# Kernel optimization log

Hardware: AMD Instinct MI355X
Metric: run time of the kernel (lower is better)

## Reference

```python
import jax, jax.numpy as jnp
import numpy as np

K = 20
EPS = 1e-5
SLOPE = 0.2

def _knn_idx(x, k):
    # x: [B, C, N] -> idx [B, N, k] of nearest neighbors (includes self)
    xx = jnp.sum(x * x, axis=1)                      # [B, N]
    inner = jnp.einsum('bcn,bcm->bnm', x, x)          # [B, N, N]
    dist = xx[:, :, None] - 2.0 * inner + xx[:, None, :]
    _, idx = jax.lax.top_k(-dist, k)                  # [B, N, k]
    return idx

def _get_attention_feature(x, k):
    # x: [B, C, N] -> [B, N, k, 2C] = cat([x_j - x_i, x_i])
    idx = _knn_idx(x, k)
    xt = jnp.transpose(x, (0, 2, 1))                  # [B, N, C]
    nbr = jax.vmap(lambda pts, ids: pts[ids])(xt, idx)  # [B, N, k, C]
    ctr = xt[:, :, None, :]                           # [B, N, 1, C]
    return jnp.concatenate([nbr - ctr, jnp.broadcast_to(ctr, nbr.shape)], axis=-1)

def _gat(feat, W, a):
    # feat: [B, N, k, 2C]; W: [2C, out_c]; a: [4, H] with H = out_c // 4
    B, N, k, _ = feat.shape
    out_c = W.shape[1]
    H = out_c // 4
    hw = jnp.einsum('bnkf,fd->bnkd', feat, W).reshape(B, N, k, H, 4)
    t = jax.nn.leaky_relu(hw, SLOPE)
    logits = jnp.einsum('bnkhd,dh->bnkh', t, a)
    w = jax.nn.softmax(logits, axis=2)                # softmax over neighbors k
    out = jnp.einsum('bnkh,bnkhd->bnhd', w, hw).reshape(B, N, out_c)
    out = jax.nn.leaky_relu(out, SLOPE)
    return jnp.transpose(out, (0, 2, 1))              # [B, out_c, N]

def _bn(x, gamma, beta):
    # BatchNorm1d in training mode (batch stats) over [B, C, N]
    mu = jnp.mean(x, axis=(0, 2), keepdims=True)
    var = jnp.var(x, axis=(0, 2), keepdims=True)
    xn = (x - mu) / jnp.sqrt(var + EPS)
    return xn * gamma[None, :, None] + beta[None, :, None]

def _layer(x, W, a, gamma, beta):
    feat = _get_attention_feature(x, K)
    h = _gat(feat, W, a)
    h = _bn(h, gamma, beta)
    return jax.nn.leaky_relu(h, SLOPE)

def setup_inputs() -> dict:
    key = jax.random.key(0)
    ks = jax.random.split(key, 10)
    dims = [(3, 64), (64, 64), (64, 128)]
    inp = {'x': jax.random.normal(ks[0], (8, 3, 2048), dtype=jnp.float32)}
    for i, (cin, cout) in enumerate(dims):
        inp[f'W{i}'] = jax.random.normal(ks[1 + 3 * i], (2 * cin, cout), dtype=jnp.float32) * 0.1
        inp[f'a{i}'] = jax.random.normal(ks[2 + 3 * i], (4, cout // 4), dtype=jnp.float32) * 0.1
        inp[f'g{i}'] = jnp.ones((cout,), dtype=jnp.float32)
        inp[f'b{i}'] = jnp.zeros((cout,), dtype=jnp.float32)
    return inp

def reference(x, W0, a0, g0, b0, W1, a1, g1, b1, W2, a2, g2, b2):
    x = _layer(x, W0, a0, g0, b0)
    x = _layer(x, W1, a1, g1, b1)
    x = _layer(x, W2, a2, g2, b2)
    return x  # [B, 128, N]
```

## Files before the change

kernel.cpp:

```cpp
#include <hip/hip_runtime.h>
#include <float.h>
#include <math.h>

#define BATCH 8
#define NPTS  2048
#define KNN   20
#define BN    (BATCH*NPTS)
#define SLOPE 0.2f
#define BNEPS 1e-5f

__global__ void xx_kernel(const float* __restrict__ x, float* __restrict__ xx, int C) {
    int p = blockIdx.x * 256 + threadIdx.x;
    int b = p >> 11, n = p & (NPTS - 1);
    const float* xb = x + (size_t)b * C * NPTS;
    float s = 0.f;
    for (int c = 0; c < C; ++c) { float v = xb[(size_t)c * NPTS + n]; s = fmaf(v, v, s); }
    xx[p] = s;
}

__device__ __forceinline__ void gload_lds16(const float* g, float* l) {
    __builtin_amdgcn_global_load_lds(
        (const __attribute__((address_space(1))) void*)g,
        (__attribute__((address_space(3))) void*)l, 16, 0, 0);
}

template<int C>
__global__ __launch_bounds__(256, 2) void knn7_kernel(const float* __restrict__ x,
                                                      const float* __restrict__ xx,
                                                      int* __restrict__ idx) {
    constexpr int ROWS = 32, CHUNK = 128, NCH = NPTS / CHUNK;
    constexpr int NST  = (C * 32 + 255) / 256;

    __shared__ __align__(16) float xrT[C][36];
    __shared__ float thrG[8][32];
    __shared__ __align__(16) union ULX {
        struct { float xc[C][CHUNK]; float dt[ROWS][129]; } s;
        struct { float v[8][KNN][ROWS]; int i[8][KNN][ROWS]; } L;
    } u;

    int t  = threadIdx.x;
    int b  = blockIdx.x >> 6;
    int r0 = (blockIdx.x & 63) * ROWS;
    const float* xb  = x  + (size_t)b * C * NPTS;
    const float* xxb = xx + (size_t)b * NPTS;

    int ty = t >> 5, tx = t & 31;
    int ty4 = ty * 4, tx4 = tx * 4;

    for (int f = t; f < ROWS * C; f += 256) {
        int r = f & 31, c = f >> 5;
        xrT[c][r] = xb[(size_t)c * NPTS + r0 + r];
    }
    thrG[ty][tx] = FLT_MAX;
#pragma unroll
    for (int k = 0; k < NST; ++k) {
        int i = t + 256 * k;
        if (i < C * 32) {
            int c = i >> 5, j = (i & 31) * 4;
            gload_lds16(xb + (size_t)c * NPTS + j, &u.s.xc[0][0] + (size_t)i * 4);
        }
    }

    float lv[KNN]; int li[KNN];
#pragma unroll
    for (int s = 0; s < KNN; ++s) { lv[s] = FLT_MAX; li[s] = 0x7fffffff; }

    __syncthreads();

    for (int ch = 0; ch < NCH; ++ch) {
        int j0 = ch * CHUNK;

        float4 a0 = {0,0,0,0}, a1 = {0,0,0,0}, a2 = {0,0,0,0}, a3 = {0,0,0,0};
#pragma unroll 4
        for (int c = 0; c < C; ++c) {
            float4 rv = *(const float4*)&xrT[c][ty4];
            float4 cv = *(const float4*)&u.s.xc[c][tx4];
            a0.x = fmaf(rv.x, cv.x, a0.x); a0.y = fmaf(rv.x, cv.y, a0.y);
            a0.z = fmaf(rv.x, cv.z, a0.z); a0.w = fmaf(rv.x, cv.w, a0.w);
            a1.x = fmaf(rv.y, cv.x, a1.x); a1.y = fmaf(rv.y, cv.y, a1.y);
            a1.z = fmaf(rv.y, cv.z, a1.z); a1.w = fmaf(rv.y, cv.w, a1.w);
            a2.x = fmaf(rv.z, cv.x, a2.x); a2.y = fmaf(rv.z, cv.y, a2.y);
            a2.z = fmaf(rv.z, cv.z, a2.z); a2.w = fmaf(rv.z, cv.w, a2.w);
            a3.x = fmaf(rv.w, cv.x, a3.x); a3.y = fmaf(rv.w, cv.y, a3.y);
            a3.z = fmaf(rv.w, cv.z, a3.z); a3.w = fmaf(rv.w, cv.w, a3.w);
        }
        {
            float4 xq = *(const float4*)&xxb[j0 + tx4];
            u.s.dt[ty4 + 0][tx4 + 0] = xq.x - 2.f * a0.x;
            u.s.dt[ty4 + 0][tx4 + 1] = xq.y - 2.f * a0.y;
            u.s.dt[ty4 + 0][tx4 + 2] = xq.z - 2.f * a0.z;
            u.s.dt[ty4 + 0][tx4 + 3] = xq.w - 2.f * a0.w;
            u.s.dt[ty4 + 1][tx4 + 0] = xq.x - 2.f * a1.x;
            u.s.dt[ty4 + 1][tx4 + 1] = xq.y - 2.f * a1.y;
            u.s.dt[ty4 + 1][tx4 + 2] = xq.z - 2.f * a1.z;
            u.s.dt[ty4 + 1][tx4 + 3] = xq.w - 2.f * a1.w;
            u.s.dt[ty4 + 2][tx4 + 0] = xq.x - 2.f * a2.x;
            u.s.dt[ty4 + 2][tx4 + 1] = xq.y - 2.f * a2.y;
            u.s.dt[ty4 + 2][tx4 + 2] = xq.z - 2.f * a2.z;
            u.s.dt[ty4 + 2][tx4 + 3] = xq.w - 2.f * a2.w;
            u.s.dt[ty4 + 3][tx4 + 0] = xq.x - 2.f * a3.x;
            u.s.dt[ty4 + 3][tx4 + 1] = xq.y - 2.f * a3.y;
            u.s.dt[ty4 + 3][tx4 + 2] = xq.z - 2.f * a3.z;
            u.s.dt[ty4 + 3][tx4 + 3] = xq.w - 2.f * a3.w;
        }
        __syncthreads();

        if (ch + 1 < NCH) {
            int j0n = j0 + CHUNK;
#pragma unroll
            for (int k = 0; k < NST; ++k) {
                int i = t + 256 * k;
                if (i < C * 32) {
                    int c = i >> 5, j = (i & 31) * 4;
                    gload_lds16(xb + (size_t)c * NPTS + j0n + j,
                                &u.s.xc[0][0] + (size_t)i * 4);
                }
            }
        }

        {
            int r = tx;
            float thr = thrG[0][r];
#pragma unroll
            for (int g = 1; g < 8; ++g) thr = fminf(thr, thrG[g][r]);

            const float* drow = &u.s.dt[r][ty * 16];
#pragma unroll
            for (int m = 0; m < 16; ++m) {
                float v = drow[m];
                if (v < lv[KNN - 1] && v <= thr) {
                    lv[KNN - 1] = v; li[KNN - 1] = j0 + ty * 16 + m;
#pragma unroll
                    for (int s = KNN - 1; s > 0; --s) {
                        if (lv[s] < lv[s - 1]) {
                            float tv = lv[s]; lv[s] = lv[s - 1]; lv[s - 1] = tv;
                            int   ti = li[s]; li[s] = li[s - 1]; li[s - 1] = ti;
                        }
                    }
                }
            }
        }
        thrG[ty][tx] = lv[KNN - 1];
        __syncthreads();
    }

    {
        int r = tx, g = ty;
#pragma unroll
        for (int s = 0; s < KNN; ++s) { u.L.v[g][s][r] = lv[s]; u.L.i[g][s][r] = li[s]; }
    }
    __syncthreads();

    if (t < ROWS) {
        int r = t;
        float hv[8]; int hi[8]; int pp[8];
#pragma unroll
        for (int g = 0; g < 8; ++g) { pp[g] = 0; hv[g] = u.L.v[g][0][r]; hi[g] = u.L.i[g][0][r]; }
        int* op = idx + (size_t)(b * NPTS + r0 + r) * KNN;
        for (int o = 0; o < KNN; ++o) {
            float bv = hv[0]; int bi = hi[0]; int bg = 0;
#pragma unroll
            for (int g = 1; g < 8; ++g)
                if (hv[g] < bv || (hv[g] == bv && hi[g] < bi)) { bv = hv[g]; bi = hi[g]; bg = g; }
            op[o] = bi;
#pragma unroll
            for (int g = 0; g < 8; ++g)
                if (bg == g) {
                    ++pp[g];
                    bool ok = pp[g] < KNN;
                    int q = ok ? pp[g] : KNN - 1;
                    float nv = u.L.v[g][q][r]; int ni = u.L.i[g][q][r];
                    hv[g] = ok ? nv : FLT_MAX;
                    hi[g] = ok ? ni : 0x7fffffff;
                }
        }
    }
}

__global__ void proj_kernel(const float* __restrict__ x, const float* __restrict__ W,
                            float* __restrict__ y, float* __restrict__ z, int C, int Cout) {
    int p = blockIdx.x;
    int b = p >> 11, n = p & (NPTS - 1);
    int j = threadIdx.x;
    __shared__ float xc[64];
    if (j < C) xc[j] = x[(size_t)b * C * NPTS + (size_t)j * NPTS + n];
    __syncthreads();
    float sy = 0.f, sz = 0.f;
    for (int c = 0; c < C; ++c) {
        float xv = xc[c];
        float wt = W[c * Cout + j];
        float wb = W[(C + c) * Cout + j];
        sy = fmaf(xv, wt, sy);
        sz = fmaf(xv, wb - wt, sz);
    }
    y[(size_t)p * Cout + j] = sy;
    z[(size_t)p * Cout + j] = sz;
}

template<int CO>
__global__ __launch_bounds__(256) void attn_kernel(const float* __restrict__ y,
                                                   const float* __restrict__ z,
                                                   const int* __restrict__ idx,
                                                   const float* __restrict__ a,
                                                   float* __restrict__ hout) {
    constexpr int NCH = CO / 64;
    constexpr int H   = CO / 4;
    int wv = threadIdx.x >> 6;
    int l  = threadIdx.x & 63;
    int p  = blockIdx.x * 4 + wv;
    int b  = p >> 11;
    float hw[NCH][KNN], lg[NCH][KNN], zv[NCH], av[NCH];
#pragma unroll
    for (int q = 0; q < NCH; ++q) {
        int c = l + 64 * q;
        zv[q] = z[(size_t)p * CO + c];
        av[q] = a[(c & 3) * H + (c >> 2)];
    }
    const int* ip = idx + (size_t)p * KNN;
#pragma unroll
    for (int j = 0; j < KNN; ++j) {
        int m = ip[j];
        const float* yr = y + ((size_t)(b * NPTS) + m) * CO;
#pragma unroll
        for (int q = 0; q < NCH; ++q) {
            int c = l + 64 * q;
            float v = yr[c] + zv[q];
            hw[q][j] = v;
            float tt = v > 0.f ? v : v * SLOPE;
            float part = tt * av[q];
            part += __shfl_xor(part, 1);
            part += __shfl_xor(part, 2);
            lg[q][j] = part;
        }
    }
#pragma unroll
    for (int q = 0; q < NCH; ++q) {
        float mx = -FLT_MAX;
#pragma unroll
        for (int j = 0; j < KNN; ++j) mx = fmaxf(mx, lg[q][j]);
        float s = 0.f;
#pragma unroll
        for (int j = 0; j < KNN; ++j) { float e = expf(lg[q][j] - mx); lg[q][j] = e; s += e; }
        float inv = 1.f / s;
        float o = 0.f;
#pragma unroll
        for (int j = 0; j < KNN; ++j) o = fmaf(lg[q][j] * inv, hw[q][j], o);
        o = o > 0.f ? o : o * SLOPE;
        int c = l + 64 * q;
        hout[(size_t)p * CO + c] = o;
    }
}

__global__ void bnstatA_kernel(const float* __restrict__ h, float* __restrict__ part, int CO) {
    __shared__ float s1[256], s2[256];
    int g = blockIdx.x, t = threadIdx.x;
    int c = t & (CO - 1), sub = t / CO;
    int nsub = 256 / CO;
    const int ppb = BN / 64;
    float a1 = 0.f, a2 = 0.f;
    for (int i = 0; i < ppb / nsub; ++i) {
        int p = g * ppb + sub + i * nsub;
        float v = h[(size_t)p * CO + c];
        a1 += v; a2 = fmaf(v, v, a2);
    }
    s1[t] = a1; s2[t] = a2;
    __syncthreads();
    if (sub == 0) {
        for (int k = 1; k < nsub; ++k) { a1 += s1[k * CO + c]; a2 += s2[k * CO + c]; }
        part[(size_t)g * CO + c]        = a1;
        part[(size_t)(64 + g) * CO + c] = a2;
    }
}

__global__ void bnstatB_kernel(const float* __restrict__ part, float* __restrict__ mu,
                               float* __restrict__ rstd, int CO) {
    int c = threadIdx.x;
    float s1 = 0.f, s2 = 0.f;
    for (int g = 0; g < 64; ++g) { s1 += part[(size_t)g * CO + c]; s2 += part[(size_t)(64 + g) * CO + c]; }
    float m   = s1 / (float)BN;
    float var = s2 / (float)BN - m * m;
    mu[c]   = m;
    rstd[c] = 1.f / sqrtf(var + BNEPS);
}

template<int CO>
__global__ __launch_bounds__(256) void bnapply_kernel(const float* __restrict__ h,
                                                      const float* __restrict__ mu,
                                                      const float* __restrict__ rstd,
                                                      const float* __restrict__ gamma,
                                                      const float* __restrict__ beta,
                                                      float* __restrict__ xout) {
    __shared__ float tile[64][CO + 1];
    int g  = blockIdx.x;
    int p0 = g * 64;
    int b  = p0 >> 11, n0 = p0 & (NPTS - 1);
    int t  = threadIdx.x;
    for (int fi = t; fi < 64 * CO; fi += 256) {
        int pt = fi / CO, c = fi % CO;
        tile[pt][c] = h[(size_t)(p0 + pt) * CO + c];
    }
    __syncthreads();
    for (int fi = t; fi < 64 * CO; fi += 256) {
        int c = fi >> 6, nn = fi & 63;
        float v = tile[nn][c];
        v = (v - mu[c]) * rstd[c] * gamma[c] + beta[c];
        v = v > 0.f ? v : v * SLOPE;
        xout[((size_t)b * CO + c) * NPTS + n0 + nn] = v;
    }
}

static void run_layer(const float* xin, const float* W, const float* a,
                      const float* gm, const float* bt, float* xout, int C, int CO,
                      float* xx, int* idx, float* y, float* z, float* h,
                      float* part, float* mu, float* rstd, hipStream_t stream) {
    xx_kernel<<<BN / 256, 256, 0, stream>>>(xin, xx, C);
    if (C == 3)
        knn7_kernel<3><<<BATCH * 64, 256, 0, stream>>>(xin, xx, idx);
    else
        knn7_kernel<64><<<BATCH * 64, 256, 0, stream>>>(xin, xx, idx);
    proj_kernel<<<BN, CO, 0, stream>>>(xin, W, y, z, C, CO);
    if (CO == 64)
        attn_kernel<64><<<BN / 4, 256, 0, stream>>>(y, z, idx, a, h);
    else
        attn_kernel<128><<<BN / 4, 256, 0, stream>>>(y, z, idx, a, h);
    bnstatA_kernel<<<64, 256, 0, stream>>>(h, part, CO);
    bnstatB_kernel<<<1, CO, 0, stream>>>(part, mu, rstd, CO);
    if (CO == 64)
        bnapply_kernel<64><<<BN / 64, 256, 0, stream>>>(h, mu, rstd, gm, bt, xout);
    else
        bnapply_kernel<128><<<BN / 64, 256, 0, stream>>>(h, mu, rstd, gm, bt, xout);
}

extern "C" void kernel_launch(void* const* d_in, const int* in_sizes, int n_in,
                              void* d_out, int out_size, void* d_ws, size_t ws_size,
                              hipStream_t stream) {
    const float* x  = (const float*)d_in[0];
    const float* W[3]  = {(const float*)d_in[1], (const float*)d_in[5], (const float*)d_in[9]};
    const float* a[3]  = {(const float*)d_in[2], (const float*)d_in[6], (const float*)d_in[10]};
    const float* gm[3] = {(const float*)d_in[3], (const float*)d_in[7], (const float*)d_in[11]};
    const float* bt[3] = {(const float*)d_in[4], (const float*)d_in[8], (const float*)d_in[12]};

    char* base = (char*)d_ws;
    size_t off = 0;
    auto carve = [&](size_t bytes) -> void* {
        void* r = base + off;
        off = (off + bytes + 255) & ~(size_t)255;
        return r;
    };
    float* xx   = (float*)carve((size_t)BN * sizeof(float));
    int*   idx  = (int*)  carve((size_t)BN * KNN * sizeof(int));
    float* y    = (float*)carve((size_t)BN * 128 * sizeof(float));
    float* z    = (float*)carve((size_t)BN * 128 * sizeof(float));
    float* h    = (float*)carve((size_t)BN * 128 * sizeof(float));
    float* part = (float*)carve((size_t)128 * 128 * sizeof(float));
    float* mu   = (float*)carve(128 * sizeof(float));
    float* rstd = (float*)carve(128 * sizeof(float));
    float* x1   = (float*)carve((size_t)BATCH * 64 * NPTS * sizeof(float));
    float* x2   = (float*)carve((size_t)BATCH * 64 * NPTS * sizeof(float));
    float* out  = (float*)d_out;

    run_layer(x,  W[0], a[0], gm[0], bt[0], x1,  3,  64, xx, idx, y, z, h, part, mu, rstd, stream);
    run_layer(x1, W[1], a[1], gm[1], bt[1], x2,  64, 64, xx, idx, y, z, h, part, mu, rstd, stream);
    run_layer(x2, W[2], a[2], gm[2], bt[2], out, 64, 128, xx, idx, y, z, h, part, mu, rstd, stream);
}
```

Before: 753.2 us.

## Split KNN candidate range across two blocks and merge partial top-k lists

```diff
diff --git a/kernel.cpp b/kernel.cpp
--- a/kernel.cpp
+++ b/kernel.cpp
@@ -25,22 +25,27 @@
 }
 
 template<int C>
-__global__ __launch_bounds__(256, 2) void knn7_kernel(const float* __restrict__ x,
+__global__ __launch_bounds__(256, 2) void knn8_kernel(const float* __restrict__ x,
                                                       const float* __restrict__ xx,
-                                                      int* __restrict__ idx) {
-    constexpr int ROWS = 32, CHUNK = 128, NCH = NPTS / CHUNK;
-    constexpr int NST  = (C * 32 + 255) / 256;
-
-    __shared__ __align__(16) float xrT[C][36];
-    __shared__ float thrG[8][32];
+                                                      float* __restrict__ pv,
+                                                      int* __restrict__ pi) {
+    constexpr int ROWS = 32, CHUNK = 128, HALF = 1024, NCH = HALF / CHUNK;
+    constexpr int CP     = (C > 32) ? 32 : C;
+    constexpr int PASSES = C / CP;
+    constexpr int NST    = (CP * 32 + 255) / 256;
+
+    __shared__ __align__(16) float xrT[C][32];
     __shared__ __align__(16) union ULX {
-        struct { float xc[C][CHUNK]; float dt[ROWS][129]; } s;
-        struct { float v[8][KNN][ROWS]; int i[8][KNN][ROWS]; } L;
+        struct { float xc[CP][CHUNK]; float dt[ROWS][129]; float thrG[8][32]; } s;
+        struct { float v[8][KNN][ROWS]; unsigned short i[8][KNN][ROWS]; } L;
     } u;
 
-    int t  = threadIdx.x;
-    int b  = blockIdx.x >> 6;
-    int r0 = (blockIdx.x & 63) * ROWS;
+    int t    = threadIdx.x;
+    int b    = blockIdx.x >> 7;
+    int tile = (blockIdx.x >> 1) & 63;
+    int half = blockIdx.x & 1;
+    int r0   = tile * ROWS;
+    int j0h  = half * HALF;
     const float* xb  = x  + (size_t)b * C * NPTS;
     const float* xxb = xx + (size_t)b * NPTS;
 
@@ -51,13 +56,13 @@
         int r = f & 31, c = f >> 5;
         xrT[c][r] = xb[(size_t)c * NPTS + r0 + r];
     }
-    thrG[ty][tx] = FLT_MAX;
+    u.s.thrG[ty][tx] = FLT_MAX;
 #pragma unroll
     for (int k = 0; k < NST; ++k) {
         int i = t + 256 * k;
-        if (i < C * 32) {
+        if (i < CP * 32) {
             int c = i >> 5, j = (i & 31) * 4;
-            gload_lds16(xb + (size_t)c * NPTS + j, &u.s.xc[0][0] + (size_t)i * 4);
+            gload_lds16(xb + (size_t)c * NPTS + j0h + j, &u.s.xc[0][0] + (size_t)i * 4);
         }
     }
 
@@ -68,11 +73,12 @@
     __syncthreads();
 
     for (int ch = 0; ch < NCH; ++ch) {
-        int j0 = ch * CHUNK;
+        int j0g = j0h + ch * CHUNK;
 
         float4 a0 = {0,0,0,0}, a1 = {0,0,0,0}, a2 = {0,0,0,0}, a3 = {0,0,0,0};
+
 #pragma unroll 4
-        for (int c = 0; c < C; ++c) {
+        for (int c = 0; c < CP; ++c) {
             float4 rv = *(const float4*)&xrT[c][ty4];
             float4 cv = *(const float4*)&u.s.xc[c][tx4];
             a0.x = fmaf(rv.x, cv.x, a0.x); a0.y = fmaf(rv.x, cv.y, a0.y);
@@ -84,8 +90,34 @@
             a3.x = fmaf(rv.w, cv.x, a3.x); a3.y = fmaf(rv.w, cv.y, a3.y);
             a3.z = fmaf(rv.w, cv.z, a3.z); a3.w = fmaf(rv.w, cv.w, a3.w);
         }
+
+        if constexpr (PASSES == 2) {
+            __syncthreads();
+#pragma unroll
+            for (int k = 0; k < NST; ++k) {
+                int i = t + 256 * k;
+                int c = i >> 5, j = (i & 31) * 4;
+                gload_lds16(xb + (size_t)(CP + c) * NPTS + j0g + j,
+                            &u.s.xc[0][0] + (size_t)i * 4);
+            }
+            __syncthreads();
+#pragma unroll 4
+            for (int c = 0; c < CP; ++c) {
+                float4 rv = *(const float4*)&xrT[CP + c][ty4];
+                float4 cv = *(const float4*)&u.s.xc[c][tx4];
+                a0.x = fmaf(rv.x, cv.x, a0.x); a0.y = fmaf(rv.x, cv.y, a0.y);
+                a0.z = fmaf(rv.x, cv.z, a0.z); a0.w = fmaf(rv.x, cv.w, a0.w);
+                a1.x = fmaf(rv.y, cv.x, a1.x); a1.y = fmaf(rv.y, cv.y, a1.y);
+                a1.z = fmaf(rv.y, cv.z, a1.z); a1.w = fmaf(rv.y, cv.w, a1.w);
+                a2.x = fmaf(rv.z, cv.x, a2.x); a2.y = fmaf(rv.z, cv.y, a2.y);
+                a2.z = fmaf(rv.z, cv.z, a2.z); a2.w = fmaf(rv.z, cv.w, a2.w);
+                a3.x = fmaf(rv.w, cv.x, a3.x); a3.y = fmaf(rv.w, cv.y, a3.y);
+                a3.z = fmaf(rv.w, cv.z, a3.z); a3.w = fmaf(rv.w, cv.w, a3.w);
+            }
+        }
+
         {
-            float4 xq = *(const float4*)&xxb[j0 + tx4];
+            float4 xq = *(const float4*)&xxb[j0g + tx4];
             u.s.dt[ty4 + 0][tx4 + 0] = xq.x - 2.f * a0.x;
             u.s.dt[ty4 + 0][tx4 + 1] = xq.y - 2.f * a0.y;
             u.s.dt[ty4 + 0][tx4 + 2] = xq.z - 2.f * a0.z;
@@ -106,11 +138,11 @@
         __syncthreads();
 
         if (ch + 1 < NCH) {
-            int j0n = j0 + CHUNK;
+            int j0n = j0g + CHUNK;
 #pragma unroll
             for (int k = 0; k < NST; ++k) {
                 int i = t + 256 * k;
-                if (i < C * 32) {
+                if (i < CP * 32) {
                     int c = i >> 5, j = (i & 31) * 4;
                     gload_lds16(xb + (size_t)c * NPTS + j0n + j,
                                 &u.s.xc[0][0] + (size_t)i * 4);
@@ -120,16 +152,16 @@
 
         {
             int r = tx;
-            float thr = thrG[0][r];
-#pragma unroll
-            for (int g = 1; g < 8; ++g) thr = fminf(thr, thrG[g][r]);
+            float thr = u.s.thrG[0][r];
+#pragma unroll
+            for (int g = 1; g < 8; ++g) thr = fminf(thr, u.s.thrG[g][r]);
 
             const float* drow = &u.s.dt[r][ty * 16];
 #pragma unroll
             for (int m = 0; m < 16; ++m) {
                 float v = drow[m];
                 if (v < lv[KNN - 1] && v <= thr) {
-                    lv[KNN - 1] = v; li[KNN - 1] = j0 + ty * 16 + m;
+                    lv[KNN - 1] = v; li[KNN - 1] = j0g + ty * 16 + m;
 #pragma unroll
                     for (int s = KNN - 1; s > 0; --s) {
                         if (lv[s] < lv[s - 1]) {
@@ -140,14 +172,17 @@
                 }
             }
         }
-        thrG[ty][tx] = lv[KNN - 1];
+        u.s.thrG[ty][tx] = lv[KNN - 1];
         __syncthreads();
     }
 
     {
         int r = tx, g = ty;
 #pragma unroll
-        for (int s = 0; s < KNN; ++s) { u.L.v[g][s][r] = lv[s]; u.L.i[g][s][r] = li[s]; }
+        for (int s = 0; s < KNN; ++s) {
+            u.L.v[g][s][r] = lv[s];
+            u.L.i[g][s][r] = (unsigned short)(li[s] & 0xFFFF);
+        }
     }
     __syncthreads();
 
@@ -156,13 +191,13 @@
         float hv[8]; int hi[8]; int pp[8];
 #pragma unroll
         for (int g = 0; g < 8; ++g) { pp[g] = 0; hv[g] = u.L.v[g][0][r]; hi[g] = u.L.i[g][0][r]; }
-        int* op = idx + (size_t)(b * NPTS + r0 + r) * KNN;
+        size_t base = ((size_t)(b * NPTS + r0 + r) * 2 + half) * KNN;
         for (int o = 0; o < KNN; ++o) {
             float bv = hv[0]; int bi = hi[0]; int bg = 0;
 #pragma unroll
             for (int g = 1; g < 8; ++g)
                 if (hv[g] < bv || (hv[g] == bv && hi[g] < bi)) { bv = hv[g]; bi = hi[g]; bg = g; }
-            op[o] = bi;
+            pv[base + o] = bv; pi[base + o] = bi;
 #pragma unroll
             for (int g = 0; g < 8; ++g)
                 if (bg == g) {
@@ -174,6 +209,22 @@
                     hi[g] = ok ? ni : 0x7fffffff;
                 }
         }
+    }
+}
+
+__global__ void knnmerge_kernel(const float* __restrict__ pv, const int* __restrict__ pi,
+                                int* __restrict__ idx) {
+    int p = blockIdx.x * 256 + threadIdx.x;
+    size_t b0 = (size_t)p * 2 * KNN, b1 = b0 + KNN;
+    int ia = 0, ib = 0;
+    int* op = idx + (size_t)p * KNN;
+    for (int o = 0; o < KNN; ++o) {
+        float va = pv[b0 + ia], vb = pv[b1 + ib];
+        int   ja = pi[b0 + ia], jb = pi[b1 + ib];
+        bool takeA = (va < vb) || (va == vb && ja < jb);
+        op[o] = takeA ? ja : jb;
+        ia += takeA ? 1 : 0;
+        ib += takeA ? 0 : 1;
     }
 }
 
@@ -311,13 +362,14 @@
 
 static void run_layer(const float* xin, const float* W, const float* a,
                       const float* gm, const float* bt, float* xout, int C, int CO,
-                      float* xx, int* idx, float* y, float* z, float* h,
+                      float* xx, float* pv, int* pi, int* idx, float* y, float* z, float* h,
                       float* part, float* mu, float* rstd, hipStream_t stream) {
     xx_kernel<<<BN / 256, 256, 0, stream>>>(xin, xx, C);
     if (C == 3)
-        knn7_kernel<3><<<BATCH * 64, 256, 0, stream>>>(xin, xx, idx);
+        knn8_kernel<3><<<BATCH * 128, 256, 0, stream>>>(xin, xx, pv, pi);
     else
-        knn7_kernel<64><<<BATCH * 64, 256, 0, stream>>>(xin, xx, idx);
+        knn8_kernel<64><<<BATCH * 128, 256, 0, stream>>>(xin, xx, pv, pi);
+    knnmerge_kernel<<<BN / 256, 256, 0, stream>>>(pv, pi, idx);
     proj_kernel<<<BN, CO, 0, stream>>>(xin, W, y, z, C, CO);
     if (CO == 64)
         attn_kernel<64><<<BN / 4, 256, 0, stream>>>(y, z, idx, a, h);
@@ -348,6 +400,8 @@
         return r;
     };
     float* xx   = (float*)carve((size_t)BN * sizeof(float));
+    float* pv   = (float*)carve((size_t)BN * 2 * KNN * sizeof(float));
+    int*   pi   = (int*)  carve((size_t)BN * 2 * KNN * sizeof(int));
     int*   idx  = (int*)  carve((size_t)BN * KNN * sizeof(int));
     float* y    = (float*)carve((size_t)BN * 128 * sizeof(float));
     float* z    = (float*)carve((size_t)BN * 128 * sizeof(float));
@@ -359,7 +413,7 @@
     float* x2   = (float*)carve((size_t)BATCH * 64 * NPTS * sizeof(float));
     float* out  = (float*)d_out;
 
-    run_layer(x,  W[0], a[0], gm[0], bt[0], x1,  3,  64, xx, idx, y, z, h, part, mu, rstd, stream);
-    run_layer(x1, W[1], a[1], gm[1], bt[1], x2,  64, 64, xx, idx, y, z, h, part, mu, rstd, stream);
-    run_layer(x2, W[2], a[2], gm[2], bt[2], out, 64, 128, xx, idx, y, z, h, part, mu, rstd, stream);
-}
+    run_layer(x,  W[0], a[0], gm[0], bt[0], x1,  3,  64, xx, pv, pi, idx, y, z, h, part, mu, rstd, stream);
+    run_layer(x1, W[1], a[1], gm[1], bt[1], x2,  64, 64, xx, pv, pi, idx, y, z, h, part, mu, rstd, stream);
+    run_layer(x2, W[2], a[2], gm[2], bt[2], out, 64, 128, xx, pv, pi, idx, y, z, h, part, mu, rstd, stream);
+}
```

Measured after the change: 780.9 us. 1.04x slower.

## Split kNN into value-only threshold pass and recompute-and-collect pass

Applied to the files above, without the earlier changes.

```diff
diff --git a/kernel.cpp b/kernel.cpp
--- a/kernel.cpp
+++ b/kernel.cpp
@@ -25,84 +25,92 @@
 }
 
 template<int C>
-__global__ __launch_bounds__(256, 2) void knn7_kernel(const float* __restrict__ x,
+__device__ __forceinline__ void dist16(const float (*xrT)[32], const float (*xc)[128],
+                                       const float* __restrict__ xxb, int j0,
+                                       int ty4, int tx4,
+                                       float4& d0, float4& d1, float4& d2, float4& d3) {
+    float4 a0 = {0,0,0,0}, a1 = {0,0,0,0}, a2 = {0,0,0,0}, a3 = {0,0,0,0};
+#pragma unroll 4
+    for (int c = 0; c < C; ++c) {
+        float4 rv = *(const float4*)&xrT[c][ty4];
+        float4 cv = *(const float4*)&xc[c][tx4];
+        a0.x = fmaf(rv.x, cv.x, a0.x); a0.y = fmaf(rv.x, cv.y, a0.y);
+        a0.z = fmaf(rv.x, cv.z, a0.z); a0.w = fmaf(rv.x, cv.w, a0.w);
+        a1.x = fmaf(rv.y, cv.x, a1.x); a1.y = fmaf(rv.y, cv.y, a1.y);
+        a1.z = fmaf(rv.y, cv.z, a1.z); a1.w = fmaf(rv.y, cv.w, a1.w);
+        a2.x = fmaf(rv.z, cv.x, a2.x); a2.y = fmaf(rv.z, cv.y, a2.y);
+        a2.z = fmaf(rv.z, cv.z, a2.z); a2.w = fmaf(rv.z, cv.w, a2.w);
+        a3.x = fmaf(rv.w, cv.x, a3.x); a3.y = fmaf(rv.w, cv.y, a3.y);
+        a3.z = fmaf(rv.w, cv.z, a3.z); a3.w = fmaf(rv.w, cv.w, a3.w);
+    }
+    float4 xq = *(const float4*)&xxb[j0 + tx4];
+    d0.x = xq.x - 2.f * a0.x; d0.y = xq.y - 2.f * a0.y;
+    d0.z = xq.z - 2.f * a0.z; d0.w = xq.w - 2.f * a0.w;
+    d1.x = xq.x - 2.f * a1.x; d1.y = xq.y - 2.f * a1.y;
+    d1.z = xq.z - 2.f * a1.z; d1.w = xq.w - 2.f * a1.w;
+    d2.x = xq.x - 2.f * a2.x; d2.y = xq.y - 2.f * a2.y;
+    d2.z = xq.z - 2.f * a2.z; d2.w = xq.w - 2.f * a2.w;
+    d3.x = xq.x - 2.f * a3.x; d3.y = xq.y - 2.f * a3.y;
+    d3.z = xq.z - 2.f * a3.z; d3.w = xq.w - 2.f * a3.w;
+}
+
+template<int C>
+__global__ __launch_bounds__(256, 2) void knn9_kernel(const float* __restrict__ x,
                                                       const float* __restrict__ xx,
                                                       int* __restrict__ idx) {
     constexpr int ROWS = 32, CHUNK = 128, NCH = NPTS / CHUNK;
     constexpr int NST  = (C * 32 + 255) / 256;
-
-    __shared__ __align__(16) float xrT[C][36];
-    __shared__ float thrG[8][32];
-    __shared__ __align__(16) union ULX {
-        struct { float xc[C][CHUNK]; float dt[ROWS][129]; } s;
-        struct { float v[8][KNN][ROWS]; int i[8][KNN][ROWS]; } L;
+    constexpr int SLOTS = 32;
+
+    __shared__ __align__(16) float xrT[C][32];
+    __shared__ float Trow[ROWS];
+    __shared__ __align__(16) union U {
+        struct P1 { float xc[C][CHUNK]; float dt[ROWS][129]; float thrG[8][32]; } p1;
+        struct PM { float mv[8][KNN][ROWS]; } pm;
+        struct P2 { float xc[C][CHUNK]; float pv[ROWS][SLOTS + 1];
+                    int pidx[ROWS][SLOTS + 1]; int cnt[ROWS]; } p2;
     } u;
 
-    int t  = threadIdx.x;
-    int b  = blockIdx.x >> 6;
-    int r0 = (blockIdx.x & 63) * ROWS;
+    const int t  = threadIdx.x;
+    const int b  = blockIdx.x >> 6;
+    const int r0 = (blockIdx.x & 63) * ROWS;
     const float* xb  = x  + (size_t)b * C * NPTS;
     const float* xxb = xx + (size_t)b * NPTS;
-
-    int ty = t >> 5, tx = t & 31;
-    int ty4 = ty * 4, tx4 = tx * 4;
+    const int ty = t >> 5, tx = t & 31;
+    const int ty4 = ty * 4, tx4 = tx * 4;
 
     for (int f = t; f < ROWS * C; f += 256) {
         int r = f & 31, c = f >> 5;
         xrT[c][r] = xb[(size_t)c * NPTS + r0 + r];
     }
-    thrG[ty][tx] = FLT_MAX;
+    u.p1.thrG[ty][tx] = FLT_MAX;
 #pragma unroll
     for (int k = 0; k < NST; ++k) {
         int i = t + 256 * k;
         if (i < C * 32) {
             int c = i >> 5, j = (i & 31) * 4;
-            gload_lds16(xb + (size_t)c * NPTS + j, &u.s.xc[0][0] + (size_t)i * 4);
-        }
-    }
-
-    float lv[KNN]; int li[KNN];
-#pragma unroll
-    for (int s = 0; s < KNN; ++s) { lv[s] = FLT_MAX; li[s] = 0x7fffffff; }
+            gload_lds16(xb + (size_t)c * NPTS + j, &u.p1.xc[0][0] + (size_t)i * 4);
+        }
+    }
+
+    float lv[KNN];
+#pragma unroll
+    for (int s = 0; s < KNN; ++s) lv[s] = FLT_MAX;
 
     __syncthreads();
 
     for (int ch = 0; ch < NCH; ++ch) {
         int j0 = ch * CHUNK;
-
-        float4 a0 = {0,0,0,0}, a1 = {0,0,0,0}, a2 = {0,0,0,0}, a3 = {0,0,0,0};
-#pragma unroll 4
-        for (int c = 0; c < C; ++c) {
-            float4 rv = *(const float4*)&xrT[c][ty4];
-            float4 cv = *(const float4*)&u.s.xc[c][tx4];
-            a0.x = fmaf(rv.x, cv.x, a0.x); a0.y = fmaf(rv.x, cv.y, a0.y);
-            a0.z = fmaf(rv.x, cv.z, a0.z); a0.w = fmaf(rv.x, cv.w, a0.w);
-            a1.x = fmaf(rv.y, cv.x, a1.x); a1.y = fmaf(rv.y, cv.y, a1.y);
-            a1.z = fmaf(rv.y, cv.z, a1.z); a1.w = fmaf(rv.y, cv.w, a1.w);
-            a2.x = fmaf(rv.z, cv.x, a2.x); a2.y = fmaf(rv.z, cv.y, a2.y);
-            a2.z = fmaf(rv.z, cv.z, a2.z); a2.w = fmaf(rv.z, cv.w, a2.w);
-            a3.x = fmaf(rv.w, cv.x, a3.x); a3.y = fmaf(rv.w, cv.y, a3.y);
-            a3.z = fmaf(rv.w, cv.z, a3.z); a3.w = fmaf(rv.w, cv.w, a3.w);
-        }
-        {
-            float4 xq = *(const float4*)&xxb[j0 + tx4];
-            u.s.dt[ty4 + 0][tx4 + 0] = xq.x - 2.f * a0.x;
-            u.s.dt[ty4 + 0][tx4 + 1] = xq.y - 2.f * a0.y;
-            u.s.dt[ty4 + 0][tx4 + 2] = xq.z - 2.f * a0.z;
-            u.s.dt[ty4 + 0][tx4 + 3] = xq.w - 2.f * a0.w;
-            u.s.dt[ty4 + 1][tx4 + 0] = xq.x - 2.f * a1.x;
-            u.s.dt[ty4 + 1][tx4 + 1] = xq.y - 2.f * a1.y;
-            u.s.dt[ty4 + 1][tx4 + 2] = xq.z - 2.f * a1.z;
-            u.s.dt[ty4 + 1][tx4 + 3] = xq.w - 2.f * a1.w;
-            u.s.dt[ty4 + 2][tx4 + 0] = xq.x - 2.f * a2.x;
-            u.s.dt[ty4 + 2][tx4 + 1] = xq.y - 2.f * a2.y;
-            u.s.dt[ty4 + 2][tx4 + 2] = xq.z - 2.f * a2.z;
-            u.s.dt[ty4 + 2][tx4 + 3] = xq.w - 2.f * a2.w;
-            u.s.dt[ty4 + 3][tx4 + 0] = xq.x - 2.f * a3.x;
-            u.s.dt[ty4 + 3][tx4 + 1] = xq.y - 2.f * a3.y;
-            u.s.dt[ty4 + 3][tx4 + 2] = xq.z - 2.f * a3.z;
-            u.s.dt[ty4 + 3][tx4 + 3] = xq.w - 2.f * a3.w;
-        }
+        float4 d0, d1, d2, d3;
+        dist16<C>(xrT, u.p1.xc, xxb, j0, ty4, tx4, d0, d1, d2, d3);
+        u.p1.dt[ty4 + 0][tx4 + 0] = d0.x; u.p1.dt[ty4 + 0][tx4 + 1] = d0.y;
+        u.p1.dt[ty4 + 0][tx4 + 2] = d0.z; u.p1.dt[ty4 + 0][tx4 + 3] = d0.w;
+        u.p1.dt[ty4 + 1][tx4 + 0] = d1.x; u.p1.dt[ty4 + 1][tx4 + 1] = d1.y;
+        u.p1.dt[ty4 + 1][tx4 + 2] = d1.z; u.p1.dt[ty4 + 1][tx4 + 3] = d1.w;
+        u.p1.dt[ty4 + 2][tx4 + 0] = d2.x; u.p1.dt[ty4 + 2][tx4 + 1] = d2.y;
+        u.p1.dt[ty4 + 2][tx4 + 2] = d2.z; u.p1.dt[ty4 + 2][tx4 + 3] = d2.w;
+        u.p1.dt[ty4 + 3][tx4 + 0] = d3.x; u.p1.dt[ty4 + 3][tx4 + 1] = d3.y;
+        u.p1.dt[ty4 + 3][tx4 + 2] = d3.z; u.p1.dt[ty4 + 3][tx4 + 3] = d3.w;
         __syncthreads();
 
         if (ch + 1 < NCH) {
@@ -113,66 +121,125 @@
                 if (i < C * 32) {
                     int c = i >> 5, j = (i & 31) * 4;
                     gload_lds16(xb + (size_t)c * NPTS + j0n + j,
-                                &u.s.xc[0][0] + (size_t)i * 4);
+                                &u.p1.xc[0][0] + (size_t)i * 4);
                 }
             }
         }
 
         {
             int r = tx;
-            float thr = thrG[0][r];
-#pragma unroll
-            for (int g = 1; g < 8; ++g) thr = fminf(thr, thrG[g][r]);
-
-            const float* drow = &u.s.dt[r][ty * 16];
+            float thr = u.p1.thrG[0][r];
+#pragma unroll
+            for (int g = 1; g < 8; ++g) thr = fminf(thr, u.p1.thrG[g][r]);
+            const float* drow = &u.p1.dt[r][ty * 16];
 #pragma unroll
             for (int m = 0; m < 16; ++m) {
                 float v = drow[m];
                 if (v < lv[KNN - 1] && v <= thr) {
-                    lv[KNN - 1] = v; li[KNN - 1] = j0 + ty * 16 + m;
+                    lv[KNN - 1] = v;
 #pragma unroll
                     for (int s = KNN - 1; s > 0; --s) {
-                        if (lv[s] < lv[s - 1]) {
-                            float tv = lv[s]; lv[s] = lv[s - 1]; lv[s - 1] = tv;
-                            int   ti = li[s]; li[s] = li[s - 1]; li[s - 1] = ti;
-                        }
+                        float lo = fminf(lv[s - 1], lv[s]);
+                        float hi = fmaxf(lv[s - 1], lv[s]);
+                        lv[s - 1] = lo; lv[s] = hi;
                     }
                 }
             }
         }
-        thrG[ty][tx] = lv[KNN - 1];
+        u.p1.thrG[ty][tx] = lv[KNN - 1];
         __syncthreads();
     }
 
+#pragma unroll
+    for (int s = 0; s < KNN; ++s) u.pm.mv[ty][s][tx] = lv[s];
+    __syncthreads();
+    if (t < ROWS) {
+        float hv[8]; int pp[8];
+#pragma unroll
+        for (int g = 0; g < 8; ++g) { pp[g] = 0; hv[g] = u.pm.mv[g][0][t]; }
+        float T = FLT_MAX;
+        for (int o = 0; o < KNN; ++o) {
+            float bv = hv[0]; int bg = 0;
+#pragma unroll
+            for (int g = 1; g < 8; ++g) if (hv[g] < bv) { bv = hv[g]; bg = g; }
+            T = bv;
+#pragma unroll
+            for (int g = 0; g < 8; ++g)
+                if (bg == g) { ++pp[g]; hv[g] = (pp[g] < KNN) ? u.pm.mv[g][pp[g]][t] : FLT_MAX; }
+        }
+        Trow[t] = T;
+    }
+    __syncthreads();
+
+    for (int f = t; f < ROWS * (SLOTS + 1); f += 256)
+        u.p2.pv[f / (SLOTS + 1)][f % (SLOTS + 1)] = FLT_MAX;
+    if (t < ROWS) u.p2.cnt[t] = 0;
+#pragma unroll
+    for (int k = 0; k < NST; ++k) {
+        int i = t + 256 * k;
+        if (i < C * 32) {
+            int c = i >> 5, j = (i & 31) * 4;
+            gload_lds16(xb + (size_t)c * NPTS + j, &u.p2.xc[0][0] + (size_t)i * 4);
+        }
+    }
+    float Tr0 = Trow[ty4 + 0], Tr1 = Trow[ty4 + 1];
+    float Tr2 = Trow[ty4 + 2], Tr3 = Trow[ty4 + 3];
+    __syncthreads();
+
+    for (int ch = 0; ch < NCH; ++ch) {
+        int j0 = ch * CHUNK;
+        float4 d0, d1, d2, d3;
+        dist16<C>(xrT, u.p2.xc, xxb, j0, ty4, tx4, d0, d1, d2, d3);
+        __syncthreads();
+
+        if (ch + 1 < NCH) {
+            int j0n = j0 + CHUNK;
+#pragma unroll
+            for (int k = 0; k < NST; ++k) {
+                int i = t + 256 * k;
+                if (i < C * 32) {
+                    int c = i >> 5, j = (i & 31) * 4;
+                    gload_lds16(xb + (size_t)c * NPTS + j0n + j,
+                                &u.p2.xc[0][0] + (size_t)i * 4);
+                }
+            }
+        }
+
+#define KNN9_EMIT(vv, ri, Tri, cj)                                         \
+        if ((vv) <= (Tri)) {                                               \
+            int sl = atomicAdd(&u.p2.cnt[ty4 + (ri)], 1);                  \
+            if (sl < SLOTS) {                                              \
+                u.p2.pv[ty4 + (ri)][sl]   = (vv);                          \
+                u.p2.pidx[ty4 + (ri)][sl] = j0 + tx4 + (cj);               \
+            }                                                              \
+        }
+        KNN9_EMIT(d0.x, 0, Tr0, 0) KNN9_EMIT(d0.y, 0, Tr0, 1)
+        KNN9_EMIT(d0.z, 0, Tr0, 2) KNN9_EMIT(d0.w, 0, Tr0, 3)
+        KNN9_EMIT(d1.x, 1, Tr1, 0) KNN9_EMIT(d1.y, 1, Tr1, 1)
+        KNN9_EMIT(d1.z, 1, Tr1, 2) KNN9_EMIT(d1.w, 1, Tr1, 3)
+        KNN9_EMIT(d2.x, 2, Tr2, 0) KNN9_EMIT(d2.y, 2, Tr2, 1)
+        KNN9_EMIT(d2.z, 2, Tr2, 2) KNN9_EMIT(d2.w, 2, Tr2, 3)
+        KNN9_EMIT(d3.x, 3, Tr3, 0) KNN9_EMIT(d3.y, 3, Tr3, 1)
+        KNN9_EMIT(d3.z, 3, Tr3, 2) KNN9_EMIT(d3.w, 3, Tr3, 3)
+#undef KNN9_EMIT
+        __syncthreads();
+    }
+
     {
-        int r = tx, g = ty;
-#pragma unroll
-        for (int s = 0; s < KNN; ++s) { u.L.v[g][s][r] = lv[s]; u.L.i[g][s][r] = li[s]; }
-    }
-    __syncthreads();
-
-    if (t < ROWS) {
-        int r = t;
-        float hv[8]; int hi[8]; int pp[8];
-#pragma unroll
-        for (int g = 0; g < 8; ++g) { pp[g] = 0; hv[g] = u.L.v[g][0][r]; hi[g] = u.L.i[g][0][r]; }
+        int r = tx;
         int* op = idx + (size_t)(b * NPTS + r0 + r) * KNN;
-        for (int o = 0; o < KNN; ++o) {
-            float bv = hv[0]; int bi = hi[0]; int bg = 0;
-#pragma unroll
-            for (int g = 1; g < 8; ++g)
-                if (hv[g] < bv || (hv[g] == bv && hi[g] < bi)) { bv = hv[g]; bi = hi[g]; bg = g; }
-            op[o] = bi;
-#pragma unroll
-            for (int g = 0; g < 8; ++g)
-                if (bg == g) {
-                    ++pp[g];
-                    bool ok = pp[g] < KNN;
-                    int q = ok ? pp[g] : KNN - 1;
-                    float nv = u.L.v[g][q][r]; int ni = u.L.i[g][q][r];
-                    hv[g] = ok ? nv : FLT_MAX;
-                    hi[g] = ok ? ni : 0x7fffffff;
+#pragma unroll
+        for (int ss = 0; ss < 4; ++ss) {
+            int s0 = ty4 + ss;
+            float v0 = u.p2.pv[r][s0]; int i0 = u.p2.pidx[r][s0];
+            if (v0 < FLT_MAX) {
+                int rank = 0;
+                for (int q = 0; q < SLOTS; ++q) {
+                    float vq = u.p2.pv[r][q]; int iq = u.p2.pidx[r][q];
+                    rank += (vq < v0 || (vq == v0 && iq < i0)) ? 1 : 0;
                 }
+                if (rank < KNN) op[rank] = i0;
+            }
         }
     }
 }
@@ -315,9 +382,9 @@
                       float* part, float* mu, float* rstd, hipStream_t stream) {
     xx_kernel<<<BN / 256, 256, 0, stream>>>(xin, xx, C);
     if (C == 3)
-        knn7_kernel<3><<<BATCH * 64, 256, 0, stream>>>(xin, xx, idx);
+        knn9_kernel<3><<<BATCH * 64, 256, 0, stream>>>(xin, xx, idx);
     else
-        knn7_kernel<64><<<BATCH * 64, 256, 0, stream>>>(xin, xx, idx);
+        knn9_kernel<64><<<BATCH * 64, 256, 0, stream>>>(xin, xx, idx);
     proj_kernel<<<BN, CO, 0, stream>>>(xin, W, y, z, C, CO);
     if (CO == 64)
         attn_kernel<64><<<BN / 4, 256, 0, stream>>>(y, z, idx, a, h);
```

Result: slower. 896.4 us (+19.0%).

## Add dedicated 3-channel KNN kernel with per-thread distance compute and double-buffered chunks

Applied to the files above, without the earlier changes.

```diff
diff --git a/kernel.cpp b/kernel.cpp
--- a/kernel.cpp
+++ b/kernel.cpp
@@ -8,6 +8,10 @@
 #define BN    (BATCH*NPTS)
 #define SLOPE 0.2f
 #define BNEPS 1e-5f
+
+__device__ __forceinline__ float f4c(const float4& v, int cc) {
+    return cc == 0 ? v.x : cc == 1 ? v.y : cc == 2 ? v.z : v.w;
+}
 
 __global__ void xx_kernel(const float* __restrict__ x, float* __restrict__ xx, int C) {
     int p = blockIdx.x * 256 + threadIdx.x;
@@ -25,9 +29,9 @@
 }
 
 template<int C>
-__global__ __launch_bounds__(256, 2) void knn7_kernel(const float* __restrict__ x,
-                                                      const float* __restrict__ xx,
-                                                      int* __restrict__ idx) {
+__global__ __launch_bounds__(256) void knn7_kernel(const float* __restrict__ x,
+                                                   const float* __restrict__ xx,
+                                                   int* __restrict__ idx) {
     constexpr int ROWS = 32, CHUNK = 128, NCH = NPTS / CHUNK;
     constexpr int NST  = (C * 32 + 255) / 256;
 
@@ -35,7 +39,7 @@
     __shared__ float thrG[8][32];
     __shared__ __align__(16) union ULX {
         struct { float xc[C][CHUNK]; float dt[ROWS][129]; } s;
-        struct { float v[8][KNN][ROWS]; int i[8][KNN][ROWS]; } L;
+        struct { float v[8][KNN][ROWS]; unsigned short i[8][KNN][ROWS]; } L;
     } u;
 
     int t  = threadIdx.x;
@@ -147,7 +151,10 @@
     {
         int r = tx, g = ty;
 #pragma unroll
-        for (int s = 0; s < KNN; ++s) { u.L.v[g][s][r] = lv[s]; u.L.i[g][s][r] = li[s]; }
+        for (int s = 0; s < KNN; ++s) {
+            u.L.v[g][s][r] = lv[s];
+            u.L.i[g][s][r] = (unsigned short)(li[s] & 0xFFFF);
+        }
     }
     __syncthreads();
 
@@ -172,6 +179,121 @@
                     float nv = u.L.v[g][q][r]; int ni = u.L.i[g][q][r];
                     hv[g] = ok ? nv : FLT_MAX;
                     hi[g] = ok ? ni : 0x7fffffff;
+                }
+        }
+    }
+}
+
+__global__ __launch_bounds__(256, 2) void knn3f_kernel(const float* __restrict__ x,
+                                                       const float* __restrict__ xx,
+                                                       int* __restrict__ idx) {
+    constexpr int ROWS = 16, CHUNK = 256, NCH = NPTS / CHUNK;
+    constexpr int G = 16;
+
+    __shared__ __align__(16) float xcb[2][3][260];
+    __shared__ float thrG[G][ROWS];
+    __shared__ __align__(16) struct LL {
+        float v[G][KNN][ROWS]; unsigned short i[G][KNN][ROWS];
+    } L;
+
+    int t  = threadIdx.x;
+    int b  = blockIdx.x >> 7;
+    int r0 = (blockIdx.x & 127) * ROWS;
+    const float* xb  = x  + (size_t)b * 3 * NPTS;
+    const float* xxb = xx + (size_t)b * NPTS;
+    int r = t & 15, g = t >> 4;
+
+    float f0 = xb[r0 + r];
+    float f1 = xb[NPTS + r0 + r];
+    float f2 = xb[2 * NPTS + r0 + r];
+    thrG[g][r] = FLT_MAX;
+
+    if (t < 192) {
+        int c = t >> 6, jq = t & 63;
+        gload_lds16(xb + (size_t)c * NPTS + jq * 4, &xcb[0][0][0] + c * 260 + jq * 4);
+    }
+
+    float lv[KNN]; int li[KNN];
+#pragma unroll
+    for (int s = 0; s < KNN; ++s) { lv[s] = FLT_MAX; li[s] = 0x7fffffff; }
+
+    __syncthreads();
+
+    int cur = 0;
+    for (int ch = 0; ch < NCH; ++ch) {
+        int j0 = ch * CHUNK;
+
+        if (ch + 1 < NCH && t < 192) {
+            int c = t >> 6, jq = t & 63;
+            gload_lds16(xb + (size_t)c * NPTS + j0 + CHUNK + jq * 4,
+                        &xcb[cur ^ 1][0][0] + c * 260 + jq * 4);
+        }
+
+        float thr = thrG[0][r];
+#pragma unroll
+        for (int q = 1; q < G; ++q) thr = fminf(thr, thrG[q][r]);
+
+        const float* c0 = &xcb[cur][0][g * 16];
+        const float* c1 = c0 + 260;
+        const float* c2 = c0 + 520;
+#pragma unroll
+        for (int mq = 0; mq < 4; ++mq) {
+            float4 xq = *(const float4*)&xxb[j0 + g * 16 + mq * 4];
+#pragma unroll
+            for (int mm = 0; mm < 4; ++mm) {
+                int m = mq * 4 + mm;
+                float acc = 0.f;
+                acc = fmaf(f0, c0[m], acc);
+                acc = fmaf(f1, c1[m], acc);
+                acc = fmaf(f2, c2[m], acc);
+                float v = f4c(xq, mm) - 2.f * acc;
+                if (v < lv[KNN - 1] && v <= thr) {
+                    lv[KNN - 1] = v; li[KNN - 1] = j0 + g * 16 + m;
+#pragma unroll
+                    for (int s = KNN - 1; s > 0; --s) {
+                        if (lv[s] < lv[s - 1]) {
+                            float tv = lv[s]; lv[s] = lv[s - 1]; lv[s - 1] = tv;
+                            int   ti = li[s]; li[s] = li[s - 1]; li[s - 1] = ti;
+                        }
+                    }
+                }
+            }
+        }
+        thrG[g][r] = lv[KNN - 1];
+        __syncthreads();
+        cur ^= 1;
+    }
+
+    {
+#pragma unroll
+        for (int s = 0; s < KNN; ++s) {
+            L.v[g][s][r] = lv[s];
+            L.i[g][s][r] = (unsigned short)(li[s] & 0xFFFF);
+        }
+    }
+    __syncthreads();
+
+    if (t < ROWS) {
+        int rr = t;
+        float hv[G]; int hi[G]; int pp[G];
+#pragma unroll
+        for (int q = 0; q < G; ++q) { pp[q] = 0; hv[q] = L.v[q][0][rr]; hi[q] = L.i[q][0][rr]; }
+        int* op = idx + (size_t)(b * NPTS + r0 + rr) * KNN;
+        for (int o = 0; o < KNN; ++o) {
+            float bv = hv[0]; int bi = hi[0]; int bg = 0;
+#pragma unroll
+            for (int q = 1; q < G; ++q)
+                if (hv[q] < bv || (hv[q] == bv && hi[q] < bi)) { bv = hv[q]; bi = hi[q]; bg = q; }
+            op[o] = bi;
+#pragma unroll
+            for (int q = 0; q < G; ++q)
+                if (bg == q) {
+                    ++pp[q];
+                    bool ok = pp[q] < KNN;
+                    int w = ok ? pp[q] : KNN - 1;
+                    float nv = L.v[q][w][rr]; int ni = L.i[q][w][rr];
+                    hv[q] = ok ? nv : FLT_MAX;
+                    hi[q] = ok ? ni : 0x7fffffff;
                 }
         }
     }
@@ -315,7 +437,7 @@
                       float* part, float* mu, float* rstd, hipStream_t stream) {
     xx_kernel<<<BN / 256, 256, 0, stream>>>(xin, xx, C);
     if (C == 3)
-        knn7_kernel<3><<<BATCH * 64, 256, 0, stream>>>(xin, xx, idx);
+        knn3f_kernel<<<BATCH * 128, 256, 0, stream>>>(xin, xx, idx);
     else
         knn7_kernel<64><<<BATCH * 64, 256, 0, stream>>>(xin, xx, idx);
     proj_kernel<<<BN, CO, 0, stream>>>(xin, W, y, z, C, CO);
```

Measured after the change: 760.7 us. No clear change (+1.0%).
